# Kernel tuning notes

Measured on AMD Instinct MI355X. Metric: run time of the kernel, lower is better.

## Reference

```python
import jax, jax.numpy as jnp
import numpy as np
import math

D_MODEL = 1024
N_HEADS = 16
D_K = D_MODEL // N_HEADS
SEQ_LEN = 2048
BATCH = 2


def setup_inputs() -> dict:
    key = jax.random.key(0)
    ks = jax.random.split(key, 5)
    X = jax.random.normal(ks[0], (BATCH, SEQ_LEN, D_MODEL), dtype=jnp.float32)
    # Linear params (torch Linear: y = x @ W.T + b). Store as [in, out] for einsum.
    sc1 = 1.0 / math.sqrt(D_MODEL)
    W_qkv = jax.random.uniform(ks[1], (D_MODEL, 3 * D_MODEL), jnp.float32, -sc1, sc1)
    b_qkv = jax.random.uniform(ks[2], (3 * D_MODEL,), jnp.float32, -sc1, sc1)
    W_out = jax.random.uniform(ks[3], (D_MODEL, D_MODEL), jnp.float32, -sc1, sc1)
    b_out = jax.random.uniform(ks[4], (D_MODEL,), jnp.float32, -sc1, sc1)
    return {"X": X, "W_qkv": W_qkv, "b_qkv": b_qkv, "W_out": W_out, "b_out": b_out}


def reference(X, W_qkv, b_qkv, W_out, b_out):
    B, S, E = X.shape
    qkv = X @ W_qkv + b_qkv                       # [B,S,3E]
    qkv = qkv.reshape(B, S, 3, N_HEADS, D_K)
    q = jnp.transpose(qkv[:, :, 0], (0, 2, 1, 3))  # [B,H,S,Dk]
    k = jnp.transpose(qkv[:, :, 1], (0, 2, 1, 3))
    v = jnp.transpose(qkv[:, :, 2], (0, 2, 1, 3))
    scores = jnp.einsum('bhqd,bhkd->bhqk', q, k) / math.sqrt(D_K)
    causal = jnp.tril(jnp.ones((S, S), dtype=bool))
    scores = jnp.where(causal[None, None], scores, -jnp.inf)
    probs = jax.nn.softmax(scores, axis=-1)
    out = jnp.einsum('bhqk,bhkd->bhqd', probs, v)  # [B,H,S,Dk]
    out = jnp.transpose(out, (0, 2, 1, 3)).reshape(B, S, E)
    return out @ W_out + b_out
```

## Files before the change

kernel.cpp:

```cpp
#include <hip/hip_runtime.h>

typedef __bf16 bf16_t;
typedef bf16_t bf16x8 __attribute__((ext_vector_type(8)));
typedef bf16_t bf16x4 __attribute__((ext_vector_type(4)));
typedef float f32x4 __attribute__((ext_vector_type(4)));

#define SEQLEN 2048
#define EMB 1024
#define NHEADS 16
#define N3 3072
#define NBATCH 2
#define NEG_INF (-__builtin_inff())
#define SC2 0.18033688011112042f

__device__ __forceinline__ void async16(bf16_t* lds, const bf16_t* g) {
    __builtin_amdgcn_global_load_lds(
        (const __attribute__((address_space(1))) void*)g,
        (__attribute__((address_space(3))) void*)lds, 16, 0, 0);
}

__global__ __launch_bounds__(256) void transpose_weights(
    const float* __restrict__ Wqkv, const float* __restrict__ Wout,
    bf16_t* __restrict__ Wqkv_t, bf16_t* __restrict__ Wout_t)
{
    __shared__ float tile[64][65];
    int bx = blockIdx.x;
    const int k0 = blockIdx.y * 64;
    const float* W; bf16_t* Wt; int N; float s;
    if (bx < 48) { W = Wqkv; Wt = Wqkv_t; N = N3;  s = (bx * 64 < EMB) ? SC2 : 1.0f; }
    else         { bx -= 48; W = Wout; Wt = Wout_t; N = EMB; s = 1.0f; }
    const int n0 = bx * 64;
    const int t = threadIdx.x;
    const int nl = t & 63, k4 = t >> 6;
#pragma unroll
    for (int i = 0; i < 16; ++i) {
        int kk = k4 + i * 4;
        tile[kk][nl] = W[(size_t)(k0 + kk) * N + n0 + nl];
    }
    __syncthreads();
    const int kl = t & 63, n4 = t >> 6;
#pragma unroll
    for (int i = 0; i < 16; ++i) {
        int nn = n4 + i * 4;
        Wt[(size_t)(n0 + nn) * EMB + k0 + kl] = (bf16_t)(tile[kl][nn] * s);
    }
}

__global__ __launch_bounds__(256) void cvt_f32_bf16(
    const float* __restrict__ in, bf16_t* __restrict__ out, int n)
{
    const int i = (blockIdx.x * 256 + threadIdx.x) * 8;
    if (i >= n) return;
    float4 a = *(const float4*)&in[i];
    float4 b = *(const float4*)&in[i + 4];
    bf16_t v[8];
    v[0] = (bf16_t)a.x; v[1] = (bf16_t)a.y; v[2] = (bf16_t)a.z; v[3] = (bf16_t)a.w;
    v[4] = (bf16_t)b.x; v[5] = (bf16_t)b.y; v[6] = (bf16_t)b.z; v[7] = (bf16_t)b.w;
    *(float4*)&out[i] = *(float4*)&v[0];
}

template<bool OUT_BF16, bool V_SPLIT>
__global__ __launch_bounds__(256) void gemm_bt_kernel(
    const bf16_t* __restrict__ A, const bf16_t* __restrict__ Bt,
    const float* __restrict__ bias, void* __restrict__ Cp,
    bf16_t* __restrict__ vt, int scale_q,
    int Mdim, int Ndim, int Kdim)
{
    __shared__ bf16_t As[128 * 32];
    __shared__ bf16_t Bs[128 * 32];
    const int nb = Ndim >> 7;
    const int cpx = gridDim.x >> 3;
    const int bid = (blockIdx.x & 7) * cpx + (blockIdx.x >> 3);
    const int bx = bid % nb, by = bid / nb;
    const int r0 = by << 7, c0 = bx << 7;
    const int t = threadIdx.x, lane = t & 63;
    const int wid = t >> 6;
    const int wm = wid >> 1, wn = wid & 1;
    const int lr = lane & 15, lg = lane >> 4;

    const int glrow = wid * 32 + (lane >> 2);
    const int glcol = (lane & 3) << 3;
    bf16_t* ldsA = &As[wid * 1024];
    bf16_t* ldsB = &Bs[wid * 1024];
    const bf16_t* gA = &A[(size_t)(r0 + glrow) * Kdim + glcol];
    const bf16_t* gB = &Bt[(size_t)(c0 + glrow) * Kdim + glcol];
    const size_t rowstep = (size_t)16 * Kdim;

    f32x4 acc[4][4] = {};
    const int KT = Kdim >> 5;
    for (int kt = 0; kt < KT; ++kt) {
        const int k0 = kt << 5;
        async16(ldsA,       gA + k0);
        async16(ldsA + 512, gA + k0 + rowstep);
        async16(ldsB,       gB + k0);
        async16(ldsB + 512, gB + k0 + rowstep);
        __syncthreads();
        bf16x8 af[4], bfm[4];
#pragma unroll
        for (int m = 0; m < 4; ++m)
            af[m] = *(const bf16x8*)&As[(wm * 64 + m * 16 + lr) * 32 + lg * 8];
#pragma unroll
        for (int n = 0; n < 4; ++n)
            bfm[n] = *(const bf16x8*)&Bs[(wn * 64 + n * 16 + lr) * 32 + lg * 8];
#pragma unroll
        for (int m = 0; m < 4; ++m)
#pragma unroll
            for (int n = 0; n < 4; ++n)
                acc[m][n] = __builtin_amdgcn_mfma_f32_16x16x32_bf16(
                    af[m], bfm[n], acc[m][n], 0, 0, 0);
        __syncthreads();
    }

    const bool vmode = V_SPLIT && (c0 >= 2 * EMB);
#pragma unroll
    for (int m = 0; m < 4; ++m) {
#pragma unroll
        for (int n = 0; n < 4; ++n) {
            const int col = c0 + wn * 64 + n * 16 + lr;
            float bval = bias[col];
            if (scale_q && col < EMB) bval *= SC2;
            if (vmode) {
                const int h = (col - 2 * EMB) >> 6, dd = col & 63;
                const int bb = r0 >> 11;
                const int sbase = (r0 & (SEQLEN - 1)) + wm * 64 + m * 16 + lg * 4;
                bf16x4 pk;
#pragma unroll
                for (int j = 0; j < 4; ++j) pk[j] = (bf16_t)(acc[m][n][j] + bval);
                *(bf16x4*)&vt[(size_t)((bb * 16 + h) * 64 + dd) * SEQLEN + sbase] = pk;
            } else {
#pragma unroll
                for (int j = 0; j < 4; ++j) {
                    const int row = r0 + wm * 64 + m * 16 + lg * 4 + j;
                    const float v = acc[m][n][j] + bval;
                    if (OUT_BF16)
                        ((bf16_t*)Cp)[(size_t)row * Ndim + col] = (bf16_t)v;
                    else
                        ((float*)Cp)[(size_t)row * Ndim + col] = v;
                }
            }
        }
    }
}

__global__ __launch_bounds__(256, 4) void attn_kernel(
    const bf16_t* __restrict__ qkv, const bf16_t* __restrict__ vt,
    bf16_t* __restrict__ attn_out)
{
    __shared__ bf16_t Kl[2][4096];
    __shared__ bf16_t Vl[2][4096];
    const int d = blockIdx.x;
    const int r = d >> 8;
    const int u = (d >> 3) & 31;
    int qt = (r & 1) ? (31 - u) : u;
    if (r & 2) qt ^= 16;
    const int bh = (d & 7) + (r << 3);
    const int b = bh >> 4, h = bh & 15;
    const int q0 = qt << 6;
    const int t = threadIdx.x, lane = t & 63, wid = t >> 6;
    const int lr = lane & 15, lg = lane >> 4;
    const int sr = t >> 2, sc16 = (t & 3) << 4;

    const int fragb0 = (lr * 128 + lg * 16) ^ ((lr & 7) << 4);
    const int fragb1 = (lr * 128 + 64 + lg * 16) ^ ((lr & 7) << 4);
    const int stb0   = (sr * 128 + sc16 * 2) ^ ((sr & 7) << 4);
    const int stb1   = (sr * 128 + sc16 * 2 + 16) ^ ((sr & 7) << 4);

    const bf16_t* kp = &qkv[(size_t)(b * SEQLEN + sr) * N3 + EMB + h * 64 + sc16];
    const bf16_t* vp = &vt[(size_t)(bh * 64 + sr) * SEQLEN + sc16];
    const size_t kstep = (size_t)64 * N3;

    const int qg = q0 + wid * 16 + lr;
    bf16x8 qa0, qa1;
    {
        const bf16_t* qb = &qkv[(size_t)(b * SEQLEN + qg) * N3 + h * 64];
        qa0 = *(const bf16x8*)&qb[lg * 8];
        qa1 = *(const bf16x8*)&qb[32 + lg * 8];
    }
    bf16x8 ones;
#pragma unroll
    for (int i = 0; i < 8; ++i) ones[i] = (bf16_t)1.0f;

    f32x4 o[4] = {};
    f32x4 ol = {};
    float m_run = NEG_INF;

    auto stK = [&](char* base, float4 a, float4 c) {
        *(float4*)(base + stb0) = a; *(float4*)(base + stb1) = c;
    };
    auto stV = [&](char* base, float4 a, float4 c) {
        float4 w0 = {a.x, a.y, c.x, c.y};
        float4 w1 = {a.z, a.w, c.z, c.w};
        *(float4*)(base + stb0) = w0; *(float4*)(base + stb1) = w1;
    };

    {
        float4 k0 = *(const float4*)kp, k1 = *(const float4*)(kp + 8);
        float4 v0 = *(const float4*)vp, v1 = *(const float4*)(vp + 8);
        stK((char*)Kl[0], k0, k1);
        stV((char*)Vl[0], v0, v1);
    }
    __syncthreads();
    int cur = 0;
    for (int kt = 0; kt <= qt; ++kt) {
        float4 nk0, nk1, nv0, nv1;
        const bool more = (kt < qt);
        if (more) {
            kp += kstep; vp += 64;
            nk0 = *(const float4*)kp; nk1 = *(const float4*)(kp + 8);
            nv0 = *(const float4*)vp; nv1 = *(const float4*)(vp + 8);
        }

        const char* Kc = (const char*)Kl[cur];
        const char* Vc = (const char*)Vl[cur];

        f32x4 sc[4] = {};
        __builtin_amdgcn_s_setprio(1);
#pragma unroll
        for (int n = 0; n < 4; ++n) {
            bf16x8 kb0 = *(const bf16x8*)(Kc + (fragb0 + n * 2048));
            bf16x8 kb1 = *(const bf16x8*)(Kc + (fragb1 + n * 2048));
            sc[n] = __builtin_amdgcn_mfma_f32_16x16x32_bf16(kb0, qa0, sc[n], 0, 0, 0);
            sc[n] = __builtin_amdgcn_mfma_f32_16x16x32_bf16(kb1, qa1, sc[n], 0, 0, 0);
        }
        __builtin_amdgcn_s_setprio(0);

        if (kt == qt) {
#pragma unroll
            for (int n = 0; n < 4; ++n)
#pragma unroll
                for (int j = 0; j < 4; ++j) {
                    const int kg = kt * 64 + n * 16 + lg * 4 + j;
                    sc[n][j] = (kg <= qg) ? sc[n][j] : NEG_INF;
                }
        }
        float mx[4];
#pragma unroll
        for (int n = 0; n < 4; ++n)
            mx[n] = fmaxf(fmaxf(fmaxf(sc[n][0], sc[n][1]), sc[n][2]), sc[n][3]);
        float pmax = fmaxf(fmaxf(fmaxf(mx[0], mx[1]), mx[2]), mx[3]);

        if (__any(pmax > m_run + 8.f)) {
            float pm = fmaxf(pmax, __shfl_xor(pmax, 16));
            pm = fmaxf(pm, __shfl_xor(pm, 32));
            const float mnew = fmaxf(m_run, pm);
            const float alpha = exp2f(m_run - mnew);
            m_run = mnew;
            float al[4];
#pragma unroll
            for (int j = 0; j < 4; ++j) al[j] = __shfl(alpha, lg * 4 + j);
#pragma unroll
            for (int dn = 0; dn < 4; ++dn)
#pragma unroll
                for (int j = 0; j < 4; ++j) o[dn][j] *= al[j];
#pragma unroll
            for (int j = 0; j < 4; ++j) ol[j] *= al[j];
        }

#pragma unroll
        for (int n = 0; n < 4; ++n)
#pragma unroll
            for (int j = 0; j < 4; ++j) sc[n][j] = exp2f(sc[n][j] - m_run);

        unsigned pk00, pk01, pk10, pk11, pk20, pk21, pk30, pk31;
        asm("v_cvt_pk_bf16_f32 %0, %1, %2" : "=v"(pk00) : "v"(sc[0][0]), "v"(sc[0][1]));
        asm("v_cvt_pk_bf16_f32 %0, %1, %2" : "=v"(pk01) : "v"(sc[0][2]), "v"(sc[0][3]));
        asm("v_cvt_pk_bf16_f32 %0, %1, %2" : "=v"(pk10) : "v"(sc[1][0]), "v"(sc[1][1]));
        asm("v_cvt_pk_bf16_f32 %0, %1, %2" : "=v"(pk11) : "v"(sc[1][2]), "v"(sc[1][3]));
        asm("v_cvt_pk_bf16_f32 %0, %1, %2" : "=v"(pk20) : "v"(sc[2][0]), "v"(sc[2][1]));
        asm("v_cvt_pk_bf16_f32 %0, %1, %2" : "=v"(pk21) : "v"(sc[2][2]), "v"(sc[2][3]));
        asm("v_cvt_pk_bf16_f32 %0, %1, %2" : "=v"(pk30) : "v"(sc[3][0]), "v"(sc[3][1]));
        asm("v_cvt_pk_bf16_f32 %0, %1, %2" : "=v"(pk31) : "v"(sc[3][2]), "v"(sc[3][3]));
        asm("v_permlane32_swap_b32 %0, %1" : "+v"(pk00), "+v"(pk10));
        asm("v_permlane32_swap_b32 %0, %1" : "+v"(pk01), "+v"(pk11));
        asm("v_permlane32_swap_b32 %0, %1" : "+v"(pk20), "+v"(pk30));
        asm("v_permlane32_swap_b32 %0, %1" : "+v"(pk21), "+v"(pk31));
        union UW { unsigned w[4]; bf16x8 v; };
        UW ua, ub;
        ua.w[0] = pk00; ua.w[1] = pk01; ua.w[2] = pk10; ua.w[3] = pk11;
        ub.w[0] = pk20; ub.w[1] = pk21; ub.w[2] = pk30; ub.w[3] = pk31;
        const bf16x8 pa0 = ua.v, pa1 = ub.v;

        __builtin_amdgcn_s_setprio(1);
#pragma unroll
        for (int dn = 0; dn < 4; ++dn) {
            bf16x8 vb0 = *(const bf16x8*)(Vc + (fragb0 + dn * 2048));
            bf16x8 vb1 = *(const bf16x8*)(Vc + (fragb1 + dn * 2048));
            o[dn] = __builtin_amdgcn_mfma_f32_16x16x32_bf16(pa0, vb0, o[dn], 0, 0, 0);
            o[dn] = __builtin_amdgcn_mfma_f32_16x16x32_bf16(pa1, vb1, o[dn], 0, 0, 0);
        }
        ol = __builtin_amdgcn_mfma_f32_16x16x32_bf16(pa0, ones, ol, 0, 0, 0);
        ol = __builtin_amdgcn_mfma_f32_16x16x32_bf16(pa1, ones, ol, 0, 0, 0);
        __builtin_amdgcn_s_setprio(0);

        if (more) {
            stK((char*)Kl[cur ^ 1], nk0, nk1);
            stV((char*)Vl[cur ^ 1], nv0, nv1);
        }
        __syncthreads();
        cur ^= 1;
    }

    float li[4];
#pragma unroll
    for (int j = 0; j < 4; ++j) li[j] = 1.0f / ol[j];
#pragma unroll
    for (int dn = 0; dn < 4; ++dn)
#pragma unroll
        for (int j = 0; j < 4; ++j) {
            const int row = b * SEQLEN + q0 + wid * 16 + lg * 4 + j;
            attn_out[(size_t)row * EMB + h * 64 + dn * 16 + lr] =
                (bf16_t)(o[dn][j] * li[j]);
        }
}

extern "C" void kernel_launch(void* const* d_in, const int* in_sizes, int n_in,
                              void* d_out, int out_size, void* d_ws, size_t ws_size,
                              hipStream_t stream)
{
    const float* X     = (const float*)d_in[0];
    const float* W_qkv = (const float*)d_in[1];
    const float* b_qkv = (const float*)d_in[2];
    const float* W_out = (const float*)d_in[3];
    const float* b_out = (const float*)d_in[4];
    float* out = (float*)d_out;

    char* ws = (char*)d_ws;
    bf16_t* Wqkv_t = (bf16_t*)ws;
    bf16_t* Wout_t = (bf16_t*)(ws + 6u * 1024 * 1024);
    bf16_t* qkv    = (bf16_t*)(ws + 8u * 1024 * 1024);
    bf16_t* attn   = (bf16_t*)(ws + 32u * 1024 * 1024);
    bf16_t* Xb     = (bf16_t*)(ws + 40u * 1024 * 1024);
    bf16_t* Vt_g   = (bf16_t*)(ws + 48u * 1024 * 1024);

    dim3 blk(256);
    transpose_weights<<<dim3(64, 16), blk, 0, stream>>>(W_qkv, W_out, Wqkv_t, Wout_t);
    cvt_f32_bf16<<<4096 * 1024 / (256 * 8), blk, 0, stream>>>(X, Xb, 4096 * 1024);

    gemm_bt_kernel<true, true><<<(4096 / 128) * (N3 / 128), blk, 0, stream>>>(
        Xb, Wqkv_t, b_qkv, (void*)qkv, Vt_g, 1, 4096, N3, EMB);

    attn_kernel<<<32 * 32, blk, 0, stream>>>(qkv, Vt_g, attn);

    gemm_bt_kernel<false, false><<<(4096 / 128) * (EMB / 128), blk, 0, stream>>>(
        attn, Wout_t, b_out, (void*)out, nullptr, 0, 4096, EMB, EMB);
}
```

Measured before the change: 119.0 us.

## Replace QKV GEMM with 256x256-tile, 8-wave, phased double-buffered pipelined kernel

```diff
diff --git a/kernel.cpp b/kernel.cpp
--- a/kernel.cpp
+++ b/kernel.cpp
@@ -59,11 +59,172 @@
     *(float4*)&out[i] = *(float4*)&v[0];
 }
 
+#define MFMA16(MLO, NLO, AF, BF)                                              \
+    _Pragma("unroll")                                                         \
+    for (int m_ = 0; m_ < 4; ++m_) {                                          \
+        _Pragma("unroll")                                                     \
+        for (int n_ = 0; n_ < 2; ++n_) {                                      \
+            acc[(MLO) + m_][(NLO) + n_] =                                     \
+                __builtin_amdgcn_mfma_f32_16x16x32_bf16(                      \
+                    AF[m_ * 2], BF[n_ * 2],                                   \
+                    acc[(MLO) + m_][(NLO) + n_], 0, 0, 0);                    \
+            acc[(MLO) + m_][(NLO) + n_] =                                     \
+                __builtin_amdgcn_mfma_f32_16x16x32_bf16(                      \
+                    AF[m_ * 2 + 1], BF[n_ * 2 + 1],                           \
+                    acc[(MLO) + m_][(NLO) + n_], 0, 0, 0);                    \
+        }                                                                     \
+    }
+#define BAR() __builtin_amdgcn_s_barrier()
+#define VMC(N)                                                                \
+    do { asm volatile("s_waitcnt vmcnt(" #N ")" ::: "memory");                \
+         __builtin_amdgcn_sched_barrier(0); } while (0)
+
 template<bool OUT_BF16, bool V_SPLIT>
+__global__ __launch_bounds__(512, 2) void gemm_8ph_kernel(
+    const bf16_t* __restrict__ A, const bf16_t* __restrict__ Bt,
+    const float* __restrict__ bias, void* __restrict__ Cp,
+    bf16_t* __restrict__ vt, int scale_q, int Ndim, int Kdim)
+{
+    __shared__ bf16_t As[2][2][8192];
+    __shared__ bf16_t Bs[2][2][8192];
+    const int nb = Ndim >> 8;
+    const int cpx = gridDim.x >> 3;
+    const int bid = (blockIdx.x & 7) * cpx + (blockIdx.x >> 3);
+    const int bx = bid % nb, by = bid / nb;
+    const int r0 = by << 8, c0 = bx << 8;
+    const int t = threadIdx.x, lane = t & 63, w = t >> 6;
+    const int wm = w >> 2, wn = w & 3;
+    const int lr = lane & 15, lg = lane >> 4;
+
+    const int rb0 = (lr * 128 + lg * 16) ^ ((lr & 7) << 4);
+    const int rb1 = (lr * 128 + 64 + lg * 16) ^ ((lr & 7) << 4);
+
+    const int gr = (w << 4) + (lane >> 3);
+    const int gcb = (((lane & 7) ^ (lane >> 3)) << 4);
+    const size_t Kb = (size_t)Kdim * 2;
+    const char* gAp = (const char*)A + (size_t)(r0 + gr) * Kb + gcb;
+    const char* gBp = (const char*)Bt + (size_t)(c0 + gr) * Kb + gcb;
+
+    auto stgA = [&](int buf, int half, int kt) {
+        const char* s = gAp + (size_t)(half << 7) * Kb + kt * 128;
+        bf16_t* d = &As[buf][half][w << 10];
+        async16(d, (const bf16_t*)s);
+        async16(d + 512, (const bf16_t*)(s + (Kb << 3)));
+    };
+    auto stgB = [&](int buf, int half, int kt) {
+        const char* s = gBp + (size_t)(half << 7) * Kb + kt * 128;
+        bf16_t* d = &Bs[buf][half][w << 10];
+        async16(d, (const bf16_t*)s);
+        async16(d + 512, (const bf16_t*)(s + (Kb << 3)));
+    };
+    auto ldA = [&](bf16x8* dst, int buf, int mlo) {
+        const char* base = (const char*)&As[buf][wm][0];
+#pragma unroll
+        for (int m_ = 0; m_ < 4; ++m_) {
+            dst[m_ * 2]     = *(const bf16x8*)(base + (mlo + m_) * 2048 + rb0);
+            dst[m_ * 2 + 1] = *(const bf16x8*)(base + (mlo + m_) * 2048 + rb1);
+        }
+    };
+    auto ldB = [&](bf16x8* dst, int buf, int nlo) {
+        const char* base = (const char*)&Bs[buf][wn >> 1][0] + ((wn & 1) << 13);
+#pragma unroll
+        for (int n_ = 0; n_ < 2; ++n_) {
+            dst[n_ * 2]     = *(const bf16x8*)(base + (nlo + n_) * 2048 + rb0);
+            dst[n_ * 2 + 1] = *(const bf16x8*)(base + (nlo + n_) * 2048 + rb1);
+        }
+    };
+
+    f32x4 acc[8][4] = {};
+    bf16x8 a0[8], a1[8], bf[4];
+
+    stgA(0, 0, 0); stgA(0, 1, 0); stgB(0, 0, 0); stgB(0, 1, 0);
+    stgA(1, 0, 1); stgA(1, 1, 1);
+    VMC(4);
+    BAR();
+
+    const int KT = Kdim >> 6;
+    const int iters = KT >> 1;
+    for (int k = 0; k < iters; ++k) {
+        const int tt = 2 * k;
+        const bool nx2 = (tt + 2 < KT), nx3 = (tt + 3 < KT);
+        const bool last = (k == iters - 1);
+        ldA(a0, 0, 0); ldB(bf, 0, 0);
+        stgB(1, 0, tt + 1);
+        BAR();
+        __builtin_amdgcn_s_setprio(1); MFMA16(0, 0, a0, bf); __builtin_amdgcn_s_setprio(0);
+        BAR();
+        ldA(a1, 0, 4);
+        stgB(1, 1, tt + 1);
+        BAR();
+        __builtin_amdgcn_s_setprio(1); MFMA16(4, 0, a1, bf); __builtin_amdgcn_s_setprio(0);
+        BAR();
+        ldB(bf, 0, 2);
+        if (nx2) stgA(0, 0, tt + 2);
+        BAR();
+        __builtin_amdgcn_s_setprio(1); MFMA16(4, 2, a1, bf); __builtin_amdgcn_s_setprio(0);
+        BAR();
+        if (nx2) stgA(0, 1, tt + 2);
+        BAR();
+        __builtin_amdgcn_s_setprio(1); MFMA16(0, 2, a0, bf); __builtin_amdgcn_s_setprio(0);
+        if (last) { VMC(0); } else { VMC(4); }
+        BAR();
+        ldA(a0, 1, 0); ldB(bf, 1, 0);
+        if (nx2) stgB(0, 0, tt + 2);
+        BAR();
+        __builtin_amdgcn_s_setprio(1); MFMA16(0, 0, a0, bf); __builtin_amdgcn_s_setprio(0);
+        BAR();
+        ldA(a1, 1, 4);
+        if (nx2) stgB(0, 1, tt + 2);
+        BAR();
+        __builtin_amdgcn_s_setprio(1); MFMA16(4, 0, a1, bf); __builtin_amdgcn_s_setprio(0);
+        BAR();
+        ldB(bf, 1, 2);
+        if (nx3) stgA(1, 0, tt + 3);
+        BAR();
+        __builtin_amdgcn_s_setprio(1); MFMA16(4, 2, a1, bf); __builtin_amdgcn_s_setprio(0);
+        BAR();
+        if (nx3) stgA(1, 1, tt + 3);
+        BAR();
+        __builtin_amdgcn_s_setprio(1); MFMA16(0, 2, a0, bf); __builtin_amdgcn_s_setprio(0);
+        if (last) { VMC(0); } else { VMC(4); }
+        BAR();
+    }
+
+    const bool vmode = V_SPLIT && (c0 >= 2 * EMB);
+#pragma unroll
+    for (int m = 0; m < 8; ++m) {
+#pragma unroll
+        for (int n = 0; n < 4; ++n) {
+            const int col = c0 + wn * 64 + n * 16 + lr;
+            float bval = bias[col];
+            if (scale_q && col < EMB) bval *= SC2;
+            if (vmode) {
+                const int h = (col - 2 * EMB) >> 6, dd = col & 63;
+                const int bb = r0 >> 11;
+                const int sbase = (r0 & (SEQLEN - 1)) + wm * 128 + m * 16 + lg * 4;
+                bf16x4 pk;
+#pragma unroll
+                for (int j = 0; j < 4; ++j) pk[j] = (bf16_t)(acc[m][n][j] + bval);
+                *(bf16x4*)&vt[(size_t)((bb * 16 + h) * 64 + dd) * SEQLEN + sbase] = pk;
+            } else {
+#pragma unroll
+                for (int j = 0; j < 4; ++j) {
+                    const int row = r0 + wm * 128 + m * 16 + lg * 4 + j;
+                    const float v = acc[m][n][j] + bval;
+                    if (OUT_BF16)
+                        ((bf16_t*)Cp)[(size_t)row * Ndim + col] = (bf16_t)v;
+                    else
+                        ((float*)Cp)[(size_t)row * Ndim + col] = v;
+                }
+            }
+        }
+    }
+}
+
+template<bool OUT_BF16>
 __global__ __launch_bounds__(256) void gemm_bt_kernel(
     const bf16_t* __restrict__ A, const bf16_t* __restrict__ Bt,
     const float* __restrict__ bias, void* __restrict__ Cp,
-    bf16_t* __restrict__ vt, int scale_q,
     int Mdim, int Ndim, int Kdim)
 {
     __shared__ bf16_t As[128 * 32];
@@ -111,32 +272,20 @@
         __syncthreads();
     }
 
-    const bool vmode = V_SPLIT && (c0 >= 2 * EMB);
 #pragma unroll
     for (int m = 0; m < 4; ++m) {
 #pragma unroll
         for (int n = 0; n < 4; ++n) {
             const int col = c0 + wn * 64 + n * 16 + lr;
-            float bval = bias[col];
-            if (scale_q && col < EMB) bval *= SC2;
-            if (vmode) {
-                const int h = (col - 2 * EMB) >> 6, dd = col & 63;
-                const int bb = r0 >> 11;
-                const int sbase = (r0 & (SEQLEN - 1)) + wm * 64 + m * 16 + lg * 4;
-                bf16x4 pk;
-#pragma unroll
-                for (int j = 0; j < 4; ++j) pk[j] = (bf16_t)(acc[m][n][j] + bval);
-                *(bf16x4*)&vt[(size_t)((bb * 16 + h) * 64 + dd) * SEQLEN + sbase] = pk;
-            } else {
-#pragma unroll
-                for (int j = 0; j < 4; ++j) {
-                    const int row = r0 + wm * 64 + m * 16 + lg * 4 + j;
-                    const float v = acc[m][n][j] + bval;
-                    if (OUT_BF16)
-                        ((bf16_t*)Cp)[(size_t)row * Ndim + col] = (bf16_t)v;
-                    else
-                        ((float*)Cp)[(size_t)row * Ndim + col] = v;
-                }
+            const float bval = bias[col];
+#pragma unroll
+            for (int j = 0; j < 4; ++j) {
+                const int row = r0 + wm * 64 + m * 16 + lg * 4 + j;
+                const float v = acc[m][n][j] + bval;
+                if (OUT_BF16)
+                    ((bf16_t*)Cp)[(size_t)row * Ndim + col] = (bf16_t)v;
+                else
+                    ((float*)Cp)[(size_t)row * Ndim + col] = v;
             }
         }
     }
@@ -336,11 +485,11 @@
     transpose_weights<<<dim3(64, 16), blk, 0, stream>>>(W_qkv, W_out, Wqkv_t, Wout_t);
     cvt_f32_bf16<<<4096 * 1024 / (256 * 8), blk, 0, stream>>>(X, Xb, 4096 * 1024);
 
-    gemm_bt_kernel<true, true><<<(4096 / 128) * (N3 / 128), blk, 0, stream>>>(
-        Xb, Wqkv_t, b_qkv, (void*)qkv, Vt_g, 1, 4096, N3, EMB);
+    gemm_8ph_kernel<true, true><<<(4096 / 256) * (N3 / 256), dim3(512), 0, stream>>>(
+        Xb, Wqkv_t, b_qkv, (void*)qkv, Vt_g, 1, N3, EMB);
 
     attn_kernel<<<32 * 32, blk, 0, stream>>>(qkv, Vt_g, attn);
 
-    gemm_bt_kernel<false, false><<<(4096 / 128) * (EMB / 128), blk, 0, stream>>>(
-        attn, Wout_t, b_out, (void*)out, nullptr, 0, 4096, EMB, EMB);
-}
+    gemm_bt_kernel<false><<<(4096 / 128) * (EMB / 128), blk, 0, stream>>>(
+        attn, Wout_t, b_out, (void*)out, 4096, EMB, EMB);
+}
```

Measured after the change: 122.4 us. +2.8%, slower.

## Fuse fp32-to-bf16 conversion of X into QKV GEMM A-tile loading

Applied to the files above, without the earlier changes.

```diff
diff --git a/kernel.cpp b/kernel.cpp
--- a/kernel.cpp
+++ b/kernel.cpp
@@ -46,22 +46,9 @@
     }
 }
 
-__global__ __launch_bounds__(256) void cvt_f32_bf16(
-    const float* __restrict__ in, bf16_t* __restrict__ out, int n)
-{
-    const int i = (blockIdx.x * 256 + threadIdx.x) * 8;
-    if (i >= n) return;
-    float4 a = *(const float4*)&in[i];
-    float4 b = *(const float4*)&in[i + 4];
-    bf16_t v[8];
-    v[0] = (bf16_t)a.x; v[1] = (bf16_t)a.y; v[2] = (bf16_t)a.z; v[3] = (bf16_t)a.w;
-    v[4] = (bf16_t)b.x; v[5] = (bf16_t)b.y; v[6] = (bf16_t)b.z; v[7] = (bf16_t)b.w;
-    *(float4*)&out[i] = *(float4*)&v[0];
-}
-
-template<bool OUT_BF16, bool V_SPLIT>
+template<bool OUT_BF16, bool V_SPLIT, bool A_F32>
 __global__ __launch_bounds__(256) void gemm_bt_kernel(
-    const bf16_t* __restrict__ A, const bf16_t* __restrict__ Bt,
+    const void* __restrict__ Ap, const bf16_t* __restrict__ Bt,
     const float* __restrict__ bias, void* __restrict__ Cp,
     bf16_t* __restrict__ vt, int scale_q,
     int Mdim, int Ndim, int Kdim)
@@ -80,21 +67,41 @@
 
     const int glrow = wid * 32 + (lane >> 2);
     const int glcol = (lane & 3) << 3;
+    bf16_t* ldsB = &Bs[wid * 1024];
+    const bf16_t* gB = &Bt[(size_t)(c0 + glrow) * Kdim + glcol];
+    const size_t rowstepB = (size_t)16 * Kdim;
+
+    const int srow = t >> 1, skk = (t & 1) << 4;
     bf16_t* ldsA = &As[wid * 1024];
-    bf16_t* ldsB = &Bs[wid * 1024];
-    const bf16_t* gA = &A[(size_t)(r0 + glrow) * Kdim + glcol];
-    const bf16_t* gB = &Bt[(size_t)(c0 + glrow) * Kdim + glcol];
-    const size_t rowstep = (size_t)16 * Kdim;
+    const bf16_t* gA16 = nullptr;
+    const float*  gA32 = nullptr;
+    if (A_F32) gA32 = &((const float*)Ap)[(size_t)(r0 + srow) * Kdim + skk];
+    else       gA16 = &((const bf16_t*)Ap)[(size_t)(r0 + glrow) * Kdim + glcol];
+
+    f32x4 pA0, pA1, pA2, pA3, pB0, pB1, pB2, pB3;
+    auto ldAf = [&](int kt, f32x4& a, f32x4& b, f32x4& c, f32x4& d) {
+        const float* s = gA32 + kt * 32;
+        a = *(const f32x4*)(s);     b = *(const f32x4*)(s + 4);
+        c = *(const f32x4*)(s + 8); d = *(const f32x4*)(s + 12);
+    };
+    auto wrA = [&](f32x4 a, f32x4 b, f32x4 c, f32x4 d) {
+        bf16_t bv[16];
+#pragma unroll
+        for (int j = 0; j < 4; ++j) {
+            bv[j]      = (bf16_t)a[j];
+            bv[4 + j]  = (bf16_t)b[j];
+            bv[8 + j]  = (bf16_t)c[j];
+            bv[12 + j] = (bf16_t)d[j];
+        }
+        *(float4*)&As[srow * 32 + skk]     = *(float4*)&bv[0];
+        *(float4*)&As[srow * 32 + skk + 8] = *(float4*)&bv[8];
+    };
 
     f32x4 acc[4][4] = {};
     const int KT = Kdim >> 5;
-    for (int kt = 0; kt < KT; ++kt) {
-        const int k0 = kt << 5;
-        async16(ldsA,       gA + k0);
-        async16(ldsA + 512, gA + k0 + rowstep);
-        async16(ldsB,       gB + k0);
-        async16(ldsB + 512, gB + k0 + rowstep);
-        __syncthreads();
+    if (A_F32) ldAf(0, pA0, pA1, pA2, pA3);
+
+    auto compute = [&]() {
         bf16x8 af[4], bfm[4];
 #pragma unroll
         for (int m = 0; m < 4; ++m)
@@ -108,7 +115,43 @@
             for (int n = 0; n < 4; ++n)
                 acc[m][n] = __builtin_amdgcn_mfma_f32_16x16x32_bf16(
                     af[m], bfm[n], acc[m][n], 0, 0, 0);
-        __syncthreads();
+    };
+
+    if (A_F32) {
+        for (int kt = 0; kt < KT; kt += 2) {
+            {
+                const int k0 = kt << 5;
+                async16(ldsB,       gB + k0);
+                async16(ldsB + 512, gB + k0 + rowstepB);
+                wrA(pA0, pA1, pA2, pA3);
+                ldAf(kt + 1, pB0, pB1, pB2, pB3);
+                __syncthreads();
+                compute();
+                __syncthreads();
+            }
+            {
+                const int k0 = (kt + 1) << 5;
+                async16(ldsB,       gB + k0);
+                async16(ldsB + 512, gB + k0 + rowstepB);
+                wrA(pB0, pB1, pB2, pB3);
+                if (kt + 2 < KT) ldAf(kt + 2, pA0, pA1, pA2, pA3);
+                __syncthreads();
+                compute();
+                __syncthreads();
+            }
+        }
+    } else {
+        const size_t rowstepA = rowstepB;
+        for (int kt = 0; kt < KT; ++kt) {
+            const int k0 = kt << 5;
+            async16(ldsA,       gA16 + k0);
+            async16(ldsA + 512, gA16 + k0 + rowstepA);
+            async16(ldsB,       gB + k0);
+            async16(ldsB + 512, gB + k0 + rowstepB);
+            __syncthreads();
+            compute();
+            __syncthreads();
+        }
     }
 
     const bool vmode = V_SPLIT && (c0 >= 2 * EMB);
@@ -329,18 +372,16 @@
     bf16_t* Wout_t = (bf16_t*)(ws + 6u * 1024 * 1024);
     bf16_t* qkv    = (bf16_t*)(ws + 8u * 1024 * 1024);
     bf16_t* attn   = (bf16_t*)(ws + 32u * 1024 * 1024);
-    bf16_t* Xb     = (bf16_t*)(ws + 40u * 1024 * 1024);
     bf16_t* Vt_g   = (bf16_t*)(ws + 48u * 1024 * 1024);
 
     dim3 blk(256);
     transpose_weights<<<dim3(64, 16), blk, 0, stream>>>(W_qkv, W_out, Wqkv_t, Wout_t);
-    cvt_f32_bf16<<<4096 * 1024 / (256 * 8), blk, 0, stream>>>(X, Xb, 4096 * 1024);
-
-    gemm_bt_kernel<true, true><<<(4096 / 128) * (N3 / 128), blk, 0, stream>>>(
-        Xb, Wqkv_t, b_qkv, (void*)qkv, Vt_g, 1, 4096, N3, EMB);
+
+    gemm_bt_kernel<true, true, true><<<(4096 / 128) * (N3 / 128), blk, 0, stream>>>(
+        (const void*)X, Wqkv_t, b_qkv, (void*)qkv, Vt_g, 1, 4096, N3, EMB);
 
     attn_kernel<<<32 * 32, blk, 0, stream>>>(qkv, Vt_g, attn);
 
-    gemm_bt_kernel<false, false><<<(4096 / 128) * (EMB / 128), blk, 0, stream>>>(
-        attn, Wout_t, b_out, (void*)out, nullptr, 0, 4096, EMB, EMB);
-}
+    gemm_bt_kernel<false, false, false><<<(4096 / 128) * (EMB / 128), blk, 0, stream>>>(
+        (const void*)attn, Wout_t, b_out, (void*)out, nullptr, 0, 4096, EMB, EMB);
+}
```

Result: slower. 145.5 us (+22.3%).

## Double GEMM K-tile to 64 with XOR-swizzled LDS layout

Applied to the files above, without the earlier changes.

```diff
diff --git a/kernel.cpp b/kernel.cpp
--- a/kernel.cpp
+++ b/kernel.cpp
@@ -66,8 +66,8 @@
     bf16_t* __restrict__ vt, int scale_q,
     int Mdim, int Ndim, int Kdim)
 {
-    __shared__ bf16_t As[128 * 32];
-    __shared__ bf16_t Bs[128 * 32];
+    __shared__ bf16_t As[128 * 64];
+    __shared__ bf16_t Bs[128 * 64];
     const int nb = Ndim >> 7;
     const int cpx = gridDim.x >> 3;
     const int bid = (blockIdx.x & 7) * cpx + (blockIdx.x >> 3);
@@ -78,30 +78,53 @@
     const int wm = wid >> 1, wn = wid & 1;
     const int lr = lane & 15, lg = lane >> 4;
 
-    const int glrow = wid * 32 + (lane >> 2);
-    const int glcol = (lane & 3) << 3;
-    bf16_t* ldsA = &As[wid * 1024];
-    bf16_t* ldsB = &Bs[wid * 1024];
-    const bf16_t* gA = &A[(size_t)(r0 + glrow) * Kdim + glcol];
-    const bf16_t* gB = &Bt[(size_t)(c0 + glrow) * Kdim + glcol];
-    const size_t rowstep = (size_t)16 * Kdim;
+    const int glrow = wid * 32 + (lane >> 3);
+    const int gsw = ((lane & 7) ^ (lane >> 3)) << 3;
+    const bf16_t* gA = &A[(size_t)(r0 + glrow) * Kdim + gsw];
+    const bf16_t* gB = &Bt[(size_t)(c0 + glrow) * Kdim + gsw];
+    bf16_t* ldsA = &As[wid * 2048];
+    bf16_t* ldsB = &Bs[wid * 2048];
+    const size_t row8 = (size_t)8 * Kdim;
+
+    const int fragb0 = (lr * 128 + lg * 16) ^ ((lr & 7) << 4);
+    const int fragb1 = (lr * 128 + 64 + lg * 16) ^ ((lr & 7) << 4);
 
     f32x4 acc[4][4] = {};
-    const int KT = Kdim >> 5;
+    const int KT = Kdim >> 6;
     for (int kt = 0; kt < KT; ++kt) {
-        const int k0 = kt << 5;
-        async16(ldsA,       gA + k0);
-        async16(ldsA + 512, gA + k0 + rowstep);
-        async16(ldsB,       gB + k0);
-        async16(ldsB + 512, gB + k0 + rowstep);
+        const bf16_t* a = gA + kt * 64;
+        const bf16_t* b = gB + kt * 64;
+        async16(ldsA,        a);
+        async16(ldsA + 512,  a + row8);
+        async16(ldsA + 1024, a + 2 * row8);
+        async16(ldsA + 1536, a + 3 * row8);
+        async16(ldsB,        b);
+        async16(ldsB + 512,  b + row8);
+        async16(ldsB + 1024, b + 2 * row8);
+        async16(ldsB + 1536, b + 3 * row8);
         __syncthreads();
+
+        const char* Ab = (const char*)As + wm * 8192;
+        const char* Bb = (const char*)Bs + wn * 8192;
         bf16x8 af[4], bfm[4];
 #pragma unroll
         for (int m = 0; m < 4; ++m)
-            af[m] = *(const bf16x8*)&As[(wm * 64 + m * 16 + lr) * 32 + lg * 8];
+            af[m] = *(const bf16x8*)(Ab + m * 2048 + fragb0);
 #pragma unroll
         for (int n = 0; n < 4; ++n)
-            bfm[n] = *(const bf16x8*)&Bs[(wn * 64 + n * 16 + lr) * 32 + lg * 8];
+            bfm[n] = *(const bf16x8*)(Bb + n * 2048 + fragb0);
+#pragma unroll
+        for (int m = 0; m < 4; ++m)
+#pragma unroll
+            for (int n = 0; n < 4; ++n)
+                acc[m][n] = __builtin_amdgcn_mfma_f32_16x16x32_bf16(
+                    af[m], bfm[n], acc[m][n], 0, 0, 0);
+#pragma unroll
+        for (int m = 0; m < 4; ++m)
+            af[m] = *(const bf16x8*)(Ab + m * 2048 + fragb1);
+#pragma unroll
+        for (int n = 0; n < 4; ++n)
+            bfm[n] = *(const bf16x8*)(Bb + n * 2048 + fragb1);
 #pragma unroll
         for (int m = 0; m < 4; ++m)
 #pragma unroll
```

After: 110.9 us. 6.9% less time.
